# Performance work log

Measured on AMD Instinct MI355X. Metric: run time of the kernel, lower is better.

## Reference

```python
import jax, jax.numpy as jnp
import numpy as np

XY_MIN, XY_MAX = -1.0, 1.0
N_BINS = 8
DIM = 16
MIN_BW = 0.001
MIN_KS = 0.001
N_TRANSFORMS = 2


def _gather_last(a, idx):
    # a: (m, dim, K*), idx: (m, dim) -> (m, dim)
    return jnp.take_along_axis(a, idx[..., None], axis=-1)[..., 0]


def _rqs_forward(x, w_u, h_u, s_u):
    """Rational quadratic spline forward + log-det-Jacobian (tfp semantics).
    x: (m, dim); w_u,h_u: (m, dim*K); s_u: (m, dim*(K-1)). Returns (y, ladJ), both (m, dim)."""
    m = x.shape[0]
    K = N_BINS
    domain = XY_MAX - XY_MIN
    c = domain - K * MIN_BW
    bw = jax.nn.softmax(w_u.reshape(m, DIM, K), axis=-1) * c + MIN_BW   # bin widths
    bh = jax.nn.softmax(h_u.reshape(m, DIM, K), axis=-1) * c + MIN_BW   # bin heights
    d_int = jax.nn.softplus(s_u.reshape(m, DIM, K - 1)) + MIN_KS        # interior knot slopes
    ones = jnp.ones((m, DIM, 1), dtype=x.dtype)
    d = jnp.concatenate([ones, d_int, ones], axis=-1)                   # (m, dim, K+1), boundary slope 1
    zero = jnp.zeros((m, DIM, 1), dtype=x.dtype)
    xk = XY_MIN + jnp.concatenate([zero, jnp.cumsum(bw, axis=-1)], axis=-1)  # (m, dim, K+1)
    yk = XY_MIN + jnp.concatenate([zero, jnp.cumsum(bh, axis=-1)], axis=-1)
    # bin search: count of interior knots <= x
    idx = jnp.clip(jnp.sum(x[..., None] >= xk[..., 1:K], axis=-1), 0, K - 1)  # (m, dim) int
    wk = _gather_last(bw, idx)
    hk = _gather_last(bh, idx)
    x0 = _gather_last(xk, idx)
    y0 = _gather_last(yk, idx)
    d0 = _gather_last(d, idx)
    d1 = _gather_last(d, idx + 1)
    sk = hk / wk
    t = (x - x0) / wk
    omt = 1.0 - t
    denom = sk + (d1 + d0 - 2.0 * sk) * t * omt
    y = y0 + hk * (sk * t * t + d0 * t * omt) / denom
    ladJ = 2.0 * jnp.log(sk) + jnp.log(d1 * t * t + 2.0 * sk * t * omt + d0 * omt * omt) - 2.0 * jnp.log(denom)
    return y, ladJ


def _shift(x, shifts, forward):
    A, B = XY_MIN, XY_MAX
    if forward:
        return jnp.mod(x + shifts - A, B - A) + A
    return jnp.mod(x - shifts - A, B - A) + A


def setup_inputs() -> dict:
    key = jax.random.key(0)
    k = jax.random.split(key, 5)
    m = 131072
    x = jax.random.uniform(k[0], (m, DIM), dtype=jnp.float32) * 2.0 - 1.0  # in [-1, 1)
    w = jax.random.normal(k[1], (N_TRANSFORMS, m, DIM * N_BINS), dtype=jnp.float32)
    h = jax.random.normal(k[2], (N_TRANSFORMS, m, DIM * N_BINS), dtype=jnp.float32)
    s = jax.random.normal(k[3], (N_TRANSFORMS, m, DIM * (N_BINS - 1)), dtype=jnp.float32)
    shifts = jax.random.uniform(k[4], (N_TRANSFORMS, m, DIM), dtype=jnp.float32)
    return {"x": x, "w": w, "h": h, "s": s, "shifts": shifts}


def reference(x, w, h, s, shifts):
    """rqs_with_periodic_shift_ forward: shift -> RQS -> unshift, per transform."""
    ladJsum = jnp.zeros_like(x)
    for i in range(N_TRANSFORMS):
        x = _shift(x, shifts[i], forward=True)
        x, ladJ = _rqs_forward(x, w[i], h[i], s[i])
        ladJsum = ladJsum + ladJ
        x = _shift(x, shifts[i], forward=False)
    return x, ladJsum
```

## Files before the change

kernel.cpp:

```cpp
#include <hip/hip_runtime.h>
#include <math.h>

#define DIMC 16
#define KB 8
#define C_SCALE 1.992f
#define MIN_BW 0.001f
#define MIN_KS 0.001f

#define LOG2E 1.44269504088896340736f
#define LN2   0.69314718055994530942f

__device__ __forceinline__ float fast_exp(float v) {
    return __builtin_amdgcn_exp2f(v * LOG2E);
}
__device__ __forceinline__ float fast_log(float v) {
    return __builtin_amdgcn_logf(v) * LN2;
}
__device__ __forceinline__ float fast_rcp(float v) {
    return __builtin_amdgcn_rcpf(v);
}

__device__ __forceinline__ float softplus_f(float v) {
    float e = fast_exp(-fabsf(v));
    return fmaxf(v, 0.0f) + fast_log(1.0f + e);
}

__global__ __launch_bounds__(256) void spline_coupling_kernel(
    const float* __restrict__ X,
    const float* __restrict__ W,
    const float* __restrict__ H,
    const float* __restrict__ S,
    const float* __restrict__ SH,
    float* __restrict__ OUT,
    int m)
{
    const int total = m * DIMC;
    const int gid = blockIdx.x * blockDim.x + threadIdx.x;
    if (gid >= total) return;
    const int row = gid >> 4;
    const int d   = gid & 15;

    float x = X[gid];
    float ladJsum = 0.0f;

    #pragma unroll
    for (int t = 0; t < 2; ++t) {
        const size_t base = (size_t)t * m + row;
        const float4* wp = (const float4*)(W + base * (DIMC * KB) + d * KB);
        const float4* hp = (const float4*)(H + base * (DIMC * KB) + d * KB);
        const float*  sp = S + base * (DIMC * (KB - 1)) + d * (KB - 1);
        const float shift = SH[base * DIMC + d];

        {
            float v = x + shift + 1.0f;
            if (v >= 2.0f) v -= 2.0f;
            x = v - 1.0f;
        }

        float4 w0 = wp[0], w1 = wp[1];
        float4 h0 = hp[0], h1 = hp[1];
        float wv[KB] = {w0.x, w0.y, w0.z, w0.w, w1.x, w1.y, w1.z, w1.w};
        float hv[KB] = {h0.x, h0.y, h0.z, h0.w, h1.x, h1.y, h1.z, h1.w};

        float mx = wv[0];
        #pragma unroll
        for (int j = 1; j < KB; ++j) mx = fmaxf(mx, wv[j]);
        float sum = 0.0f;
        #pragma unroll
        for (int j = 0; j < KB; ++j) { wv[j] = fast_exp(wv[j] - mx); sum += wv[j]; }
        float inv = C_SCALE * fast_rcp(sum);
        #pragma unroll
        for (int j = 0; j < KB; ++j) wv[j] = wv[j] * inv + MIN_BW;

        mx = hv[0];
        #pragma unroll
        for (int j = 1; j < KB; ++j) mx = fmaxf(mx, hv[j]);
        sum = 0.0f;
        #pragma unroll
        for (int j = 0; j < KB; ++j) { hv[j] = fast_exp(hv[j] - mx); sum += hv[j]; }
        inv = C_SCALE * fast_rcp(sum);
        #pragma unroll
        for (int j = 0; j < KB; ++j) hv[j] = hv[j] * inv + MIN_BW;

        int   idx = 0;
        float xk = -1.0f, yk = -1.0f;
        float x0 = -1.0f, y0 = -1.0f;
        float wk = wv[0], hk = hv[0];
        #pragma unroll
        for (int j = 1; j < KB; ++j) {
            xk += wv[j - 1];
            yk += hv[j - 1];
            bool ge = (x >= xk);
            idx = ge ? j     : idx;
            x0  = ge ? xk    : x0;
            y0  = ge ? yk    : y0;
            wk  = ge ? wv[j] : wk;
            hk  = ge ? hv[j] : hk;
        }

        int i0 = idx - 1; if (i0 < 0) i0 = 0;
        int i1 = idx;     if (i1 > KB - 2) i1 = KB - 2;
        float s0 = sp[i0];
        float s1 = sp[i1];
        float d0 = (idx == 0)      ? 1.0f : softplus_f(s0) + MIN_KS;
        float d1 = (idx == KB - 1) ? 1.0f : softplus_f(s1) + MIN_KS;

        float rwk = fast_rcp(wk);
        float sk  = hk * rwk;
        float tt  = (x - x0) * rwk;
        float omt = 1.0f - tt;
        float a2  = d1 + d0 - 2.0f * sk;
        float den = sk + a2 * tt * omt;
        float rden = fast_rcp(den);
        float y   = y0 + hk * (sk * tt * tt + d0 * tt * omt) * rden;
        float num = d1 * tt * tt + 2.0f * sk * tt * omt + d0 * omt * omt;
        float skr = sk * rden;
        ladJsum += fast_log(skr * skr * num);

        {
            float v = y - shift + 1.0f;
            if (v < 0.0f)  v += 2.0f;
            if (v >= 2.0f) v -= 2.0f;
            x = v - 1.0f;
        }
    }

    OUT[gid] = x;
    OUT[(size_t)total + gid] = ladJsum;
}

extern "C" void kernel_launch(void* const* d_in, const int* in_sizes, int n_in,
                              void* d_out, int out_size, void* d_ws, size_t ws_size,
                              hipStream_t stream) {
    const int total = in_sizes[0];
    const int m = total / DIMC;
    const float* X  = (const float*)d_in[0];
    const float* W  = (const float*)d_in[1];
    const float* H  = (const float*)d_in[2];
    const float* S  = (const float*)d_in[3];
    const float* SH = (const float*)d_in[4];
    float* OUT = (float*)d_out;

    const int block = 256;
    const int grid = (total + block - 1) / block;
    spline_coupling_kernel<<<grid, block, 0, stream>>>(X, W, H, S, SH, OUT, m);
}
```

Measured before the change: 366.8 us.

## Stage W/H/S through LDS with coalesced loads and transposed planes

Each block now cooperatively loads its 16 rows of W, H and S with contiguous coalesced global reads, then writes them into padded, transposed LDS planes. Each thread reads its bin parameters from LDS. Previously each thread read two strided float4s for W and H plus two scattered S elements. The goal is full coalescing and reading all of S once in a streamed pattern. The cost is LDS traffic, two barriers per transform, and index arithmetic. S is now read in full, where before only two elements per thread were fetched, although at sector granularity most of it was likely fetched anyway.

Measured after the change: 369.7 us. No clear change (+0.8%).

```diff
diff --git a/kernel.cpp b/kernel.cpp
--- a/kernel.cpp
+++ b/kernel.cpp
@@ -3,6 +3,10 @@
 
 #define DIMC 16
 #define KB 8
+#define ROWS 16
+#define BLOCK 256
+#define PLANE 257
+#define SPLANE 259
 #define C_SCALE 1.992f
 #define MIN_BW 0.001f
 #define MIN_KS 0.001f
@@ -19,13 +23,12 @@
 __device__ __forceinline__ float fast_rcp(float v) {
     return __builtin_amdgcn_rcpf(v);
 }
-
 __device__ __forceinline__ float softplus_f(float v) {
     float e = fast_exp(-fabsf(v));
     return fmaxf(v, 0.0f) + fast_log(1.0f + e);
 }
 
-__global__ __launch_bounds__(256) void spline_coupling_kernel(
+__global__ __launch_bounds__(BLOCK) void spline_coupling_kernel(
     const float* __restrict__ X,
     const float* __restrict__ W,
     const float* __restrict__ H,
@@ -34,22 +37,61 @@
     float* __restrict__ OUT,
     int m)
 {
-    const int total = m * DIMC;
-    const int gid = blockIdx.x * blockDim.x + threadIdx.x;
-    if (gid >= total) return;
-    const int row = gid >> 4;
-    const int d   = gid & 15;
+    __shared__ float w_lds[KB * PLANE];
+    __shared__ float h_lds[KB * PLANE];
+    __shared__ float s_lds[(KB - 1) * SPLANE];
 
-    float x = X[gid];
+    const int tid  = threadIdx.x;
+    const int row0 = blockIdx.x * ROWS;
+    const int rows = min(ROWS, m - row0);
+    const int nelem = rows * DIMC;
+    const bool active = tid < nelem;
+    const int gid = row0 * DIMC + tid;
+
+    float x = active ? X[gid] : 0.0f;
     float ladJsum = 0.0f;
 
-    #pragma unroll
     for (int t = 0; t < 2; ++t) {
-        const size_t base = (size_t)t * m + row;
-        const float4* wp = (const float4*)(W + base * (DIMC * KB) + d * KB);
-        const float4* hp = (const float4*)(H + base * (DIMC * KB) + d * KB);
-        const float*  sp = S + base * (DIMC * (KB - 1)) + d * (KB - 1);
-        const float shift = SH[base * DIMC + d];
+        const size_t rbase = (size_t)t * m + row0;
+        const float4* wg = (const float4*)(W + rbase * (DIMC * KB));
+        const float4* hg = (const float4*)(H + rbase * (DIMC * KB));
+        const float*  sg = S + rbase * (DIMC * (KB - 1));
+
+        __syncthreads();
+
+        #pragma unroll
+        for (int u = 0; u < 2; ++u) {
+            int f4 = tid + u * BLOCK;
+            if (f4 < (rows * DIMC * KB) / 4) {
+                float4 wq = wg[f4];
+                float4 hq = hg[f4];
+                int flat = f4 << 2;
+                int a = ((flat >> 7) << 4) | ((flat >> 3) & 15);
+                int j = flat & 7;
+                w_lds[(j + 0) * PLANE + a] = wq.x;
+                w_lds[(j + 1) * PLANE + a] = wq.y;
+                w_lds[(j + 2) * PLANE + a] = wq.z;
+                w_lds[(j + 3) * PLANE + a] = wq.w;
+                h_lds[(j + 0) * PLANE + a] = hq.x;
+                h_lds[(j + 1) * PLANE + a] = hq.y;
+                h_lds[(j + 2) * PLANE + a] = hq.z;
+                h_lds[(j + 3) * PLANE + a] = hq.w;
+            }
+        }
+        #pragma unroll
+        for (int k = 0; k < 7; ++k) {
+            int flat = tid + k * BLOCK;
+            if (flat < rows * 112) {
+                float sv = sg[flat];
+                int r = flat / 112;
+                int rem = flat - r * 112;
+                int d = rem / 7;
+                int j = rem - d * 7;
+                s_lds[j * SPLANE + r * DIMC + d] = sv;
+            }
+        }
+        float shift = active ? SH[rbase * DIMC + tid] : 0.0f;
+        __syncthreads();
 
         {
             float v = x + shift + 1.0f;
@@ -57,10 +99,12 @@
             x = v - 1.0f;
         }
 
-        float4 w0 = wp[0], w1 = wp[1];
-        float4 h0 = hp[0], h1 = hp[1];
-        float wv[KB] = {w0.x, w0.y, w0.z, w0.w, w1.x, w1.y, w1.z, w1.w};
-        float hv[KB] = {h0.x, h0.y, h0.z, h0.w, h1.x, h1.y, h1.z, h1.w};
+        float wv[KB], hv[KB];
+        #pragma unroll
+        for (int j = 0; j < KB; ++j) {
+            wv[j] = w_lds[j * PLANE + tid];
+            hv[j] = h_lds[j * PLANE + tid];
+        }
 
         float mx = wv[0];
         #pragma unroll
@@ -100,8 +144,8 @@
 
         int i0 = idx - 1; if (i0 < 0) i0 = 0;
         int i1 = idx;     if (i1 > KB - 2) i1 = KB - 2;
-        float s0 = sp[i0];
-        float s1 = sp[i1];
+        float s0 = s_lds[i0 * SPLANE + tid];
+        float s1 = s_lds[i1 * SPLANE + tid];
         float d0 = (idx == 0)      ? 1.0f : softplus_f(s0) + MIN_KS;
         float d1 = (idx == KB - 1) ? 1.0f : softplus_f(s1) + MIN_KS;
 
@@ -125,8 +169,10 @@
         }
     }
 
-    OUT[gid] = x;
-    OUT[(size_t)total + gid] = ladJsum;
+    if (active) {
+        OUT[gid] = x;
+        OUT[(size_t)m * DIMC + gid] = ladJsum;
+    }
 }
 
 extern "C" void kernel_launch(void* const* d_in, const int* in_sizes, int n_in,
@@ -141,7 +187,6 @@
     const float* SH = (const float*)d_in[4];
     float* OUT = (float*)d_out;
 
-    const int block = 256;
-    const int grid = (total + block - 1) / block;
-    spline_coupling_kernel<<<grid, block, 0, stream>>>(X, W, H, S, SH, OUT, m);
+    const int grid = (m + ROWS - 1) / ROWS;
+    spline_coupling_kernel<<<grid, BLOCK, 0, stream>>>(X, W, H, S, SH, OUT, m);
 }
```
